# Optimization experiments

Hardware: AMD Instinct MI355X
Metric: run time of the kernel (lower is better)

The kernel has to match this reference:

```python
import jax, jax.numpy as jnp
import numpy as np

B, S, D, H, E, K = 4, 2048, 1024, 2048, 8, 2


def setup_inputs() -> dict:
    key = jax.random.key(0)
    ks = jax.random.split(key, 5)
    x = jax.random.normal(ks[0], (B, S, D), dtype=jnp.float32)
    Wr = jax.random.normal(ks[1], (D, E), dtype=jnp.float32) * 0.02  # router weight
    w1 = jax.random.normal(ks[2], (E, D, H), dtype=jnp.float32) * 0.02  # gate proj per expert
    w3 = jax.random.normal(ks[3], (E, D, H), dtype=jnp.float32) * 0.02  # up proj per expert
    w2 = jax.random.normal(ks[4], (E, H, D), dtype=jnp.float32) * 0.02  # down proj per expert
    return {"x": x, "Wr": Wr, "w1": w1, "w2": w2, "w3": w3}


def reference(x, Wr, w1, w2, w3):
    b, s, d = x.shape
    e = Wr.shape[1]
    flat = x.reshape(b * s, d)                      # [T, D]
    logits = flat @ Wr                              # [T, E]
    probs = jax.nn.softmax(logits, axis=-1)
    vals, idx = jax.lax.top_k(probs, K)             # [T, K]
    weights = vals / jnp.sum(vals, axis=-1, keepdims=True)
    onehot = jax.nn.one_hot(idx, e, dtype=flat.dtype)   # [T, K, E]
    cw = jnp.einsum('tke,tk->te', onehot, weights)      # combine weight per (token, expert)

    # naive dense: every expert computes every token, masked by combine weights
    out = jnp.zeros_like(flat)
    for ei in range(e):  # fixed small structural loop over experts
        h = jax.nn.silu(flat @ w1[ei]) * (flat @ w3[ei])   # [T, H]
        out = out + (h @ w2[ei]) * cw[:, ei:ei + 1]

    # aux load-balancing loss (usage uses any() over top-k slots, as in torch code)
    usage = (onehot.sum(axis=1) > 0).astype(flat.dtype).mean(axis=0)  # [E]
    prob_mass = probs.mean(axis=0)                                     # [E]
    aux_loss = e * jnp.sum(usage * prob_mass)
    return out.reshape(b, s, d), aux_loss
```

## Files before the change

### kernel.cpp

```cpp
#include <hip/hip_runtime.h>
#include <hip/hip_bf16.h>
#include <cstdint>
#include <cstddef>

#define T_TOK 8192
#define DIM   1024
#define HID   2048
#define NE    8
#define CAP   2816

typedef __attribute__((ext_vector_type(8))) short bf16x8;
typedef __attribute__((ext_vector_type(4))) float f32x4;
using bf16 = __hip_bfloat16;

__device__ __forceinline__ void gload16(const bf16* g, bf16* l) {
    __builtin_amdgcn_global_load_lds(
        (const __attribute__((address_space(1))) unsigned int*)(g),
        (__attribute__((address_space(3))) unsigned int*)(l), 16, 0, 0);
}
__device__ __forceinline__ float b2f(unsigned short u) {
    return __uint_as_float(((unsigned int)u) << 16);
}

__global__ void k_convert_x(const float* __restrict__ x, bf16* __restrict__ xb) {
    int i = (blockIdx.x * blockDim.x + threadIdx.x) * 4;
    float4 v = *(const float4*)(x + i);
    bf16 o[4] = {__float2bfloat16(v.x), __float2bfloat16(v.y),
                 __float2bfloat16(v.z), __float2bfloat16(v.w)};
    *(uint2*)(xb + i) = *(const uint2*)o;
}

__global__ __launch_bounds__(256) void k_transpose_bf16(const float* __restrict__ in,
                                                        bf16* __restrict__ out, int R, int C) {
    __shared__ float tile[64][65];
    int e = blockIdx.y;
    int ct = C >> 6;
    int r0 = (blockIdx.x / ct) << 6;
    int c0 = (blockIdx.x % ct) << 6;
    const float* src = in + (size_t)e * R * C;
    bf16* dst = out + (size_t)e * R * C;
    int s = threadIdx.x & 15, g = threadIdx.x >> 4;
#pragma unroll
    for (int j = 0; j < 4; ++j) {
        int row = j * 16 + g;
        float4 v = *(const float4*)(src + (size_t)(r0 + row) * C + c0 + s * 4);
        tile[row][s * 4 + 0] = v.x; tile[row][s * 4 + 1] = v.y;
        tile[row][s * 4 + 2] = v.z; tile[row][s * 4 + 3] = v.w;
    }
    __syncthreads();
#pragma unroll
    for (int j = 0; j < 4; ++j) {
        int c = j * 16 + g;
        int r = s * 4;
        bf16 o[4] = {__float2bfloat16(tile[r][c]),     __float2bfloat16(tile[r + 1][c]),
                     __float2bfloat16(tile[r + 2][c]), __float2bfloat16(tile[r + 3][c])};
        *(uint2*)(dst + (size_t)(c0 + c) * R + r0 + r) = *(const uint2*)o;
    }
}

__global__ __launch_bounds__(256) void k_logits(const float* __restrict__ x,
                                                const float* __restrict__ Wr,
                                                float* __restrict__ logits) {
    __shared__ float wl[NE][DIM];
    for (int o = threadIdx.x; o < NE * DIM; o += 256) {
        int e = o >> 10, d = o & (DIM - 1);
        wl[e][d] = Wr[d * NE + e];
    }
    __syncthreads();
    int wid = threadIdx.x >> 6, lane = threadIdx.x & 63;
    int t = blockIdx.x * 4 + wid;
    const float* xr = x + (size_t)t * DIM;
    double acc[NE];
#pragma unroll
    for (int e = 0; e < NE; ++e) acc[e] = 0.0;
    for (int i = 0; i < DIM / 64; ++i) {
        float xv = xr[i * 64 + lane];
#pragma unroll
        for (int e = 0; e < NE; ++e)
            acc[e] += (double)xv * (double)wl[e][i * 64 + lane];
    }
#pragma unroll
    for (int e = 0; e < NE; ++e) {
        double v = acc[e];
        for (int m = 32; m >= 1; m >>= 1) v += __shfl_xor(v, m);
        if (lane == 0) logits[t * NE + e] = (float)v;
    }
}

__global__ __launch_bounds__(256) void k_route(const float* __restrict__ logits,
                                               int* counts, int* seg_tok, float* seg_w,
                                               int* slotpos, float* probsum) {
    int t = blockIdx.x * 256 + threadIdx.x;
    float l[NE];
#pragma unroll
    for (int e = 0; e < NE; ++e) l[e] = logits[t * NE + e];
    float mx = l[0];
#pragma unroll
    for (int e = 1; e < NE; ++e) mx = fmaxf(mx, l[e]);
    float p[NE], s = 0.f;
#pragma unroll
    for (int e = 0; e < NE; ++e) { p[e] = expf(l[e] - mx); s += p[e]; }
    float inv = 1.f / s;
#pragma unroll
    for (int e = 0; e < NE; ++e) p[e] *= inv;
    int e0 = 0; float v0 = p[0];
#pragma unroll
    for (int e = 1; e < NE; ++e) if (p[e] > v0) { v0 = p[e]; e0 = e; }
    int e1 = -1; float v1 = -1.f;
#pragma unroll
    for (int e = 0; e < NE; ++e) if (e != e0 && p[e] > v1) { v1 = p[e]; e1 = e; }
    float wsum = v0 + v1;
    float w0 = v0 / wsum, w1 = v1 / wsum;

    int lane = threadIdx.x & 63, wid = threadIdx.x >> 6;
    __shared__ float ps[4][NE];
#pragma unroll
    for (int e = 0; e < NE; ++e) {
        float v = p[e];
        for (int m = 32; m >= 1; m >>= 1) v += __shfl_xor(v, m);
        if (lane == 0) ps[wid][e] = v;
    }
    __syncthreads();
    if (threadIdx.x < NE) {
        float v = ps[0][threadIdx.x] + ps[1][threadIdx.x] + ps[2][threadIdx.x] + ps[3][threadIdx.x];
        atomicAdd(&probsum[threadIdx.x], v);
    }
    for (int slot = 0; slot < 2; ++slot) {
        int   e  = slot ? e1 : e0;
        float wv = slot ? w1 : w0;
#pragma unroll
        for (int ex = 0; ex < NE; ++ex) {
            unsigned long long m = __ballot(e == ex);
            if (e == ex) {
                int leader = __ffsll(m) - 1;
                int base = 0;
                if (lane == leader) base = atomicAdd(&counts[ex], __popcll(m));
                base = __shfl(base, leader);
                int pos = base + (int)__popcll(m & ((1ull << lane) - 1ull));
                if (pos < CAP) {
                    seg_tok[ex * CAP + pos] = t;
                    seg_w[ex * CAP + pos]  = wv;
                    slotpos[2 * t + slot]  = ex * CAP + pos;
                } else {
                    slotpos[2 * t + slot]  = -1;
                }
            }
        }
    }
}

__global__ __launch_bounds__(256, 2) void k_gemm1(const bf16* __restrict__ xb,
                                                  const bf16* __restrict__ w1t,
                                                  const bf16* __restrict__ w3t,
                                                  const int* __restrict__ counts,
                                                  const int* __restrict__ seg_tok,
                                                  bf16* __restrict__ h) {
    __shared__ __align__(16) bf16 As[128 * 64];
    __shared__ __align__(16) bf16 Bg[128 * 64];
    __shared__ __align__(16) bf16 Bu[128 * 64];
    __shared__ int toks[128];
    const int NT = HID / 128;
    int flat = blockIdx.y * gridDim.x + blockIdx.x;
    int cpx  = (gridDim.x * NE) >> 3;
    int swz  = (flat & 7) * cpx + (flat >> 3);
    int e    = swz / gridDim.x;
    int tile = swz % gridDim.x;
    int mtile = tile / NT, ntile = tile % NT;
    int cnt = counts[e]; if (cnt > CAP) cnt = CAP;
    if (mtile * 128 >= cnt) return;

    int tx = threadIdx.x;
    if (tx < 128) {
        int slot = mtile * 128 + tx;
        toks[tx] = seg_tok[e * CAP + (slot < cnt ? slot : 0)];
    }
    __syncthreads();

    int lane = tx & 63, w = tx >> 6;
    const bf16 *ap[4], *gp[4], *up[4];
    bf16 *al[4], *gl[4], *ul[4];
#pragma unroll
    for (int i = 0; i < 4; ++i) {
        int seg = w * 4 + i;
        int r = seg * 8 + (lane >> 3);
        int co = (lane & 7) * 8;
        ap[i] = xb  + (size_t)toks[r] * DIM + co;
        gp[i] = w1t + ((size_t)e * HID + ntile * 128 + r) * DIM + co;
        up[i] = w3t + ((size_t)e * HID + ntile * 128 + r) * DIM + co;
        al[i] = As + seg * 512; gl[i] = Bg + seg * 512; ul[i] = Bu + seg * 512;
    }

    f32x4 zero4 = {0.f, 0.f, 0.f, 0.f};
    f32x4 accg[4][4], accu[4][4];
#pragma unroll
    for (int m = 0; m < 4; ++m)
#pragma unroll
        for (int n = 0; n < 4; ++n) { accg[m][n] = zero4; accu[m][n] = zero4; }
    int wr = w >> 1, wc = w & 1;

    for (int k0 = 0; k0 < DIM; k0 += 64) {
#pragma unroll
        for (int i = 0; i < 4; ++i) {
            gload16(ap[i] + k0, al[i]);
            gload16(gp[i] + k0, gl[i]);
            gload16(up[i] + k0, ul[i]);
        }
        __syncthreads();
#pragma unroll
        for (int ks = 0; ks < 2; ++ks) {
            bf16x8 af[4];
#pragma unroll
            for (int m = 0; m < 4; ++m)
                af[m] = *(const bf16x8*)(As + (wr * 64 + m * 16 + (lane & 15)) * 64 + ks * 32 + (lane >> 4) * 8);
#pragma unroll
            for (int n = 0; n < 4; ++n) {
                bf16x8 bgf = *(const bf16x8*)(Bg + (wc * 64 + n * 16 + (lane & 15)) * 64 + ks * 32 + (lane >> 4) * 8);
                bf16x8 buf_ = *(const bf16x8*)(Bu + (wc * 64 + n * 16 + (lane & 15)) * 64 + ks * 32 + (lane >> 4) * 8);
#pragma unroll
                for (int m = 0; m < 4; ++m) {
                    accg[m][n] = __builtin_amdgcn_mfma_f32_16x16x32_bf16(af[m], bgf, accg[m][n], 0, 0, 0);
                    accu[m][n] = __builtin_amdgcn_mfma_f32_16x16x32_bf16(af[m], buf_, accu[m][n], 0, 0, 0);
                }
            }
        }
        __syncthreads();
    }
    bf16* hdst = h + ((size_t)e * CAP + (size_t)mtile * 128) * HID + ntile * 128;
#pragma unroll
    for (int m = 0; m < 4; ++m)
#pragma unroll
        for (int n = 0; n < 4; ++n)
#pragma unroll
            for (int r = 0; r < 4; ++r) {
                int row = wr * 64 + m * 16 + (lane >> 4) * 4 + r;
                int col = wc * 64 + n * 16 + (lane & 15);
                float gg = accg[m][n][r], uu = accu[m][n][r];
                float hv = gg / (1.f + __expf(-gg)) * uu;
                hdst[(size_t)row * HID + col] = __float2bfloat16(hv);
            }
}

__global__ __launch_bounds__(256, 2) void k_gemm2(const bf16* __restrict__ h,
                                                  const bf16* __restrict__ w2t,
                                                  const int* __restrict__ counts,
                                                  const float* __restrict__ seg_w,
                                                  bf16* __restrict__ ybuf) {
    __shared__ __align__(16) bf16 As[128 * 64];
    __shared__ __align__(16) bf16 Bs[128 * 64];
    __shared__ float wts[128];
    const int NT = DIM / 128;
    int flat = blockIdx.y * gridDim.x + blockIdx.x;
    int cpx  = (gridDim.x * NE) >> 3;
    int swz  = (flat & 7) * cpx + (flat >> 3);
    int e    = swz / gridDim.x;
    int tile = swz % gridDim.x;
    int mtile = tile / NT, ntile = tile % NT;
    int cnt = counts[e]; if (cnt > CAP) cnt = CAP;
    if (mtile * 128 >= cnt) return;

    int tx = threadIdx.x;
    if (tx < 128) {
        int slot = mtile * 128 + tx;
        wts[tx] = (slot < cnt) ? seg_w[e * CAP + slot] : 0.f;
    }
    __syncthreads();

    int lane = tx & 63, w = tx >> 6;
    const bf16 *ap[4], *bp[4];
    bf16 *al[4], *bl[4];
#pragma unroll
    for (int i = 0; i < 4; ++i) {
        int seg = w * 4 + i;
        int r = seg * 8 + (lane >> 3);
        int co = (lane & 7) * 8;
        ap[i] = h   + ((size_t)e * CAP + mtile * 128 + r) * HID + co;
        bp[i] = w2t + ((size_t)e * DIM + ntile * 128 + r) * HID + co;
        al[i] = As + seg * 512; bl[i] = Bs + seg * 512;
    }

    f32x4 zero4 = {0.f, 0.f, 0.f, 0.f};
    f32x4 acc[4][4];
#pragma unroll
    for (int m = 0; m < 4; ++m)
#pragma unroll
        for (int n = 0; n < 4; ++n) acc[m][n] = zero4;
    int wr = w >> 1, wc = w & 1;

    for (int k0 = 0; k0 < HID; k0 += 64) {
#pragma unroll
        for (int i = 0; i < 4; ++i) {
            gload16(ap[i] + k0, al[i]);
            gload16(bp[i] + k0, bl[i]);
        }
        __syncthreads();
#pragma unroll
        for (int ks = 0; ks < 2; ++ks) {
            bf16x8 af[4];
#pragma unroll
            for (int m = 0; m < 4; ++m)
                af[m] = *(const bf16x8*)(As + (wr * 64 + m * 16 + (lane & 15)) * 64 + ks * 32 + (lane >> 4) * 8);
#pragma unroll
            for (int n = 0; n < 4; ++n) {
                bf16x8 b = *(const bf16x8*)(Bs + (wc * 64 + n * 16 + (lane & 15)) * 64 + ks * 32 + (lane >> 4) * 8);
#pragma unroll
                for (int m = 0; m < 4; ++m)
                    acc[m][n] = __builtin_amdgcn_mfma_f32_16x16x32_bf16(af[m], b, acc[m][n], 0, 0, 0);
            }
        }
        __syncthreads();
    }
    bf16* ydst = ybuf + ((size_t)e * CAP + (size_t)mtile * 128) * DIM + ntile * 128;
#pragma unroll
    for (int m = 0; m < 4; ++m)
#pragma unroll
        for (int n = 0; n < 4; ++n)
#pragma unroll
            for (int r = 0; r < 4; ++r) {
                int row = wr * 64 + m * 16 + (lane >> 4) * 4 + r;
                int col = wc * 64 + n * 16 + (lane & 15);
                ydst[(size_t)row * DIM + col] = __float2bfloat16(acc[m][n][r] * wts[row]);
            }
}

__global__ __launch_bounds__(256) void k_combine(const bf16* __restrict__ yb,
                                                 const int* __restrict__ slotpos,
                                                 float* __restrict__ out) {
    int t = blockIdx.x;
    int s0 = slotpos[2 * t], s1 = slotpos[2 * t + 1];
    int d = threadIdx.x * 4;
    float4 a = {0.f, 0.f, 0.f, 0.f};
    if (s0 >= 0) {
        ushort4 v = *(const ushort4*)(yb + (size_t)s0 * DIM + d);
        a.x += b2f(v.x); a.y += b2f(v.y); a.z += b2f(v.z); a.w += b2f(v.w);
    }
    if (s1 >= 0) {
        ushort4 v = *(const ushort4*)(yb + (size_t)s1 * DIM + d);
        a.x += b2f(v.x); a.y += b2f(v.y); a.z += b2f(v.z); a.w += b2f(v.w);
    }
    *(float4*)(out + (size_t)t * DIM + d) = a;
}

__global__ void k_aux(const int* __restrict__ counts, const float* __restrict__ probsum,
                      float* __restrict__ outaux) {
    if (threadIdx.x == 0 && blockIdx.x == 0) {
        float s = 0.f;
        for (int e = 0; e < NE; ++e)
            s += ((float)counts[e] / (float)T_TOK) * (probsum[e] / (float)T_TOK);
        *outaux = (float)NE * s;
    }
}

extern "C" void kernel_launch(void* const* d_in, const int* in_sizes, int n_in,
                              void* d_out, int out_size, void* d_ws, size_t ws_size,
                              hipStream_t stream) {
    const float* x  = (const float*)d_in[0];
    const float* Wr = (const float*)d_in[1];
    const float* w1 = (const float*)d_in[2];
    const float* w2 = (const float*)d_in[3];
    const float* w3 = (const float*)d_in[4];
    float* out = (float*)d_out;

    char* ws = (char*)d_ws;
    size_t off = 0;
    auto alloc = [&](size_t bytes) { void* p = ws + off; off += (bytes + 255) & ~(size_t)255; return p; };
    bf16*  xb      = (bf16*)alloc((size_t)T_TOK * DIM * 2);
    bf16*  w1t     = (bf16*)alloc((size_t)NE * HID * DIM * 2);
    bf16*  w3t     = (bf16*)alloc((size_t)NE * HID * DIM * 2);
    bf16*  w2t     = (bf16*)alloc((size_t)NE * DIM * HID * 2);
    bf16*  hbuf    = (bf16*)alloc((size_t)NE * CAP * HID * 2);
    float* logits  = (float*)alloc((size_t)T_TOK * NE * 4);
    int*   counts  = (int*)alloc(256);
    int*   segtok  = (int*)alloc((size_t)NE * CAP * 4);
    float* segw    = (float*)alloc((size_t)NE * CAP * 4);
    int*   slotpos = (int*)alloc((size_t)T_TOK * 2 * 4);
    float* probsum = (float*)alloc(256);
    bf16*  ybuf    = w1t;
    (void)ws_size; (void)in_sizes; (void)n_in;

    hipMemsetAsync(counts, 0, 256, stream);
    hipMemsetAsync(probsum, 0, 256, stream);

    k_convert_x<<<T_TOK * DIM / 4 / 256, 256, 0, stream>>>(x, xb);
    dim3 gt1((DIM / 64) * (HID / 64), NE);
    k_transpose_bf16<<<gt1, 256, 0, stream>>>(w1, w1t, DIM, HID);
    k_transpose_bf16<<<gt1, 256, 0, stream>>>(w3, w3t, DIM, HID);
    dim3 gt2((HID / 64) * (DIM / 64), NE);
    k_transpose_bf16<<<gt2, 256, 0, stream>>>(w2, w2t, HID, DIM);

    k_logits<<<T_TOK / 4, 256, 0, stream>>>(x, Wr, logits);
    k_route<<<T_TOK / 256, 256, 0, stream>>>(logits, counts, segtok, segw, slotpos, probsum);

    dim3 g1((CAP / 128) * (HID / 128), NE);
    k_gemm1<<<g1, 256, 0, stream>>>(xb, w1t, w3t, counts, segtok, hbuf);
    dim3 g2((CAP / 128) * (DIM / 128), NE);
    k_gemm2<<<g2, 256, 0, stream>>>(hbuf, w2t, counts, segw, ybuf);

    k_combine<<<T_TOK, 256, 0, stream>>>(ybuf, slotpos, out);
    k_aux<<<1, 64, 0, stream>>>(counts, probsum, out + (size_t)T_TOK * DIM);
}
```

Baseline: 439.2 us.

## Rewrite expert GEMMs with 3-stage LDS pipeline, swizzled tiles, 512-thread blocks

```diff
diff --git a/kernel.cpp b/kernel.cpp
--- a/kernel.cpp
+++ b/kernel.cpp
@@ -9,6 +9,8 @@
 #define NE    8
 #define CAP   2816
 
+#define SLOT  24576
+
 typedef __attribute__((ext_vector_type(8))) short bf16x8;
 typedef __attribute__((ext_vector_type(4))) float f32x4;
 using bf16 = __hip_bfloat16;
@@ -21,6 +23,10 @@
 __device__ __forceinline__ float b2f(unsigned short u) {
     return __uint_as_float(((unsigned int)u) << 16);
 }
+#define MFMA16(a, b, c) __builtin_amdgcn_mfma_f32_16x16x32_bf16((a), (b), (c), 0, 0, 0)
+#define BARRIER() asm volatile("s_barrier" ::: "memory")
+#define WAITVM6() asm volatile("s_waitcnt vmcnt(6)" ::: "memory")
+#define WAITVM0() asm volatile("s_waitcnt vmcnt(0)" ::: "memory")
 
 __global__ void k_convert_x(const float* __restrict__ x, bf16* __restrict__ xb) {
     int i = (blockIdx.x * blockDim.x + threadIdx.x) * 4;
@@ -149,177 +155,227 @@
     }
 }
 
-__global__ __launch_bounds__(256, 2) void k_gemm1(const bf16* __restrict__ xb,
+__global__ __launch_bounds__(512, 2) void k_gemm1(const bf16* __restrict__ xb,
                                                   const bf16* __restrict__ w1t,
                                                   const bf16* __restrict__ w3t,
                                                   const int* __restrict__ counts,
                                                   const int* __restrict__ seg_tok,
                                                   bf16* __restrict__ h) {
-    __shared__ __align__(16) bf16 As[128 * 64];
-    __shared__ __align__(16) bf16 Bg[128 * 64];
-    __shared__ __align__(16) bf16 Bu[128 * 64];
-    __shared__ int toks[128];
-    const int NT = HID / 128;
+    __shared__ __align__(16) bf16 lds[3 * SLOT];
+    __shared__ int toks[256];
+    const int NTL = HID / 64;
     int flat = blockIdx.y * gridDim.x + blockIdx.x;
     int cpx  = (gridDim.x * NE) >> 3;
     int swz  = (flat & 7) * cpx + (flat >> 3);
     int e    = swz / gridDim.x;
     int tile = swz % gridDim.x;
-    int mtile = tile / NT, ntile = tile % NT;
+    int mtile = tile / NTL, ntile = tile % NTL;
     int cnt = counts[e]; if (cnt > CAP) cnt = CAP;
-    if (mtile * 128 >= cnt) return;
-
-    int tx = threadIdx.x;
-    if (tx < 128) {
-        int slot = mtile * 128 + tx;
-        toks[tx] = seg_tok[e * CAP + (slot < cnt ? slot : 0)];
+    if (mtile * 256 >= cnt) return;
+
+    int tx = threadIdx.x, lane = tx & 63, wid = tx >> 6;
+    for (int i = tx; i < 256; i += 512) {
+        int slot = mtile * 256 + i;
+        toks[i] = seg_tok[e * CAP + (slot < cnt ? slot : 0)];
     }
     __syncthreads();
 
-    int lane = tx & 63, w = tx >> 6;
-    const bf16 *ap[4], *gp[4], *up[4];
-    bf16 *al[4], *gl[4], *ul[4];
-#pragma unroll
-    for (int i = 0; i < 4; ++i) {
-        int seg = w * 4 + i;
-        int r = seg * 8 + (lane >> 3);
-        int co = (lane & 7) * 8;
-        ap[i] = xb  + (size_t)toks[r] * DIM + co;
-        gp[i] = w1t + ((size_t)e * HID + ntile * 128 + r) * DIM + co;
-        up[i] = w3t + ((size_t)e * HID + ntile * 128 + r) * DIM + co;
-        al[i] = As + seg * 512; gl[i] = Bg + seg * 512; ul[i] = Bu + seg * 512;
-    }
-
+    int l3 = lane >> 3, l7 = lane & 7;
+    int swzco = (l7 ^ l3) << 3;
+    const bf16* ap0 = xb + (size_t)toks[  0 + wid * 8 + l3] * DIM + swzco;
+    const bf16* ap1 = xb + (size_t)toks[ 64 + wid * 8 + l3] * DIM + swzco;
+    const bf16* ap2 = xb + (size_t)toks[128 + wid * 8 + l3] * DIM + swzco;
+    const bf16* ap3 = xb + (size_t)toks[192 + wid * 8 + l3] * DIM + swzco;
+    const bf16* bgp = w1t + ((size_t)e * HID + ntile * 64 + wid * 8 + l3) * DIM + swzco;
+    const bf16* bup = w3t + ((size_t)e * HID + ntile * 64 + wid * 8 + l3) * DIM + swzco;
+    int wbase = wid * 512;
+
+    f32x4 accg[4][2], accu[4][2];
     f32x4 zero4 = {0.f, 0.f, 0.f, 0.f};
-    f32x4 accg[4][4], accu[4][4];
 #pragma unroll
     for (int m = 0; m < 4; ++m)
 #pragma unroll
-        for (int n = 0; n < 4; ++n) { accg[m][n] = zero4; accu[m][n] = zero4; }
-    int wr = w >> 1, wc = w & 1;
-
-    for (int k0 = 0; k0 < DIM; k0 += 64) {
-#pragma unroll
-        for (int i = 0; i < 4; ++i) {
-            gload16(ap[i] + k0, al[i]);
-            gload16(gp[i] + k0, gl[i]);
-            gload16(up[i] + k0, ul[i]);
-        }
-        __syncthreads();
-#pragma unroll
-        for (int ks = 0; ks < 2; ++ks) {
-            bf16x8 af[4];
-#pragma unroll
-            for (int m = 0; m < 4; ++m)
-                af[m] = *(const bf16x8*)(As + (wr * 64 + m * 16 + (lane & 15)) * 64 + ks * 32 + (lane >> 4) * 8);
-#pragma unroll
-            for (int n = 0; n < 4; ++n) {
-                bf16x8 bgf = *(const bf16x8*)(Bg + (wc * 64 + n * 16 + (lane & 15)) * 64 + ks * 32 + (lane >> 4) * 8);
-                bf16x8 buf_ = *(const bf16x8*)(Bu + (wc * 64 + n * 16 + (lane & 15)) * 64 + ks * 32 + (lane >> 4) * 8);
-#pragma unroll
-                for (int m = 0; m < 4; ++m) {
-                    accg[m][n] = __builtin_amdgcn_mfma_f32_16x16x32_bf16(af[m], bgf, accg[m][n], 0, 0, 0);
-                    accu[m][n] = __builtin_amdgcn_mfma_f32_16x16x32_bf16(af[m], buf_, accu[m][n], 0, 0, 0);
-                }
-            }
-        }
-        __syncthreads();
-    }
-    bf16* hdst = h + ((size_t)e * CAP + (size_t)mtile * 128) * HID + ntile * 128;
+        for (int n = 0; n < 2; ++n) { accg[m][n] = zero4; accu[m][n] = zero4; }
+
+    int wm = wid >> 1, wn = wid & 1;
+    int l15 = lane & 15, lh = lane >> 4;
+
+#define G1_STAGE_A(ss, ko) do { \
+        gload16(ap0 + (ko), lds + (ss) + 0 * 4096 + wbase); \
+        gload16(ap1 + (ko), lds + (ss) + 1 * 4096 + wbase); \
+        gload16(ap2 + (ko), lds + (ss) + 2 * 4096 + wbase); } while (0)
+#define G1_STAGE_B(ss, ko) do { \
+        gload16(ap3 + (ko), lds + (ss) + 3 * 4096 + wbase); \
+        gload16(bgp + (ko), lds + (ss) + 16384 + wbase); \
+        gload16(bup + (ko), lds + (ss) + 20480 + wbase); } while (0)
+#define G1_PHASE(cs, ph) do { \
+        int cex = ((((ph) << 2) + lh) ^ l7) << 3; \
+        bf16x8 a0 = *(const bf16x8*)(lds + (cs) + (wm * 64 +  0 + l15) * 64 + cex); \
+        bf16x8 a1 = *(const bf16x8*)(lds + (cs) + (wm * 64 + 16 + l15) * 64 + cex); \
+        bf16x8 a2 = *(const bf16x8*)(lds + (cs) + (wm * 64 + 32 + l15) * 64 + cex); \
+        bf16x8 a3 = *(const bf16x8*)(lds + (cs) + (wm * 64 + 48 + l15) * 64 + cex); \
+        bf16x8 g0 = *(const bf16x8*)(lds + (cs) + 16384 + (wn * 32 +  0 + l15) * 64 + cex); \
+        bf16x8 g1 = *(const bf16x8*)(lds + (cs) + 16384 + (wn * 32 + 16 + l15) * 64 + cex); \
+        bf16x8 u0 = *(const bf16x8*)(lds + (cs) + 20480 + (wn * 32 +  0 + l15) * 64 + cex); \
+        bf16x8 u1 = *(const bf16x8*)(lds + (cs) + 20480 + (wn * 32 + 16 + l15) * 64 + cex); \
+        __builtin_amdgcn_s_setprio(1); \
+        accg[0][0] = MFMA16(a0, g0, accg[0][0]); accg[1][0] = MFMA16(a1, g0, accg[1][0]); \
+        accg[2][0] = MFMA16(a2, g0, accg[2][0]); accg[3][0] = MFMA16(a3, g0, accg[3][0]); \
+        accg[0][1] = MFMA16(a0, g1, accg[0][1]); accg[1][1] = MFMA16(a1, g1, accg[1][1]); \
+        accg[2][1] = MFMA16(a2, g1, accg[2][1]); accg[3][1] = MFMA16(a3, g1, accg[3][1]); \
+        accu[0][0] = MFMA16(a0, u0, accu[0][0]); accu[1][0] = MFMA16(a1, u0, accu[1][0]); \
+        accu[2][0] = MFMA16(a2, u0, accu[2][0]); accu[3][0] = MFMA16(a3, u0, accu[3][0]); \
+        accu[0][1] = MFMA16(a0, u1, accu[0][1]); accu[1][1] = MFMA16(a1, u1, accu[1][1]); \
+        accu[2][1] = MFMA16(a2, u1, accu[2][1]); accu[3][1] = MFMA16(a3, u1, accu[3][1]); \
+        __builtin_amdgcn_s_setprio(0); } while (0)
+
+    G1_STAGE_A(0, 0);    G1_STAGE_B(0, 0);
+    G1_STAGE_A(SLOT, 64); G1_STAGE_B(SLOT, 64);
+
+    const int NT = DIM / 64;
+    int cs = 0, ss = 2 * SLOT, ko = 128;
+#pragma unroll 1
+    for (int T = 0; T < NT; ++T) {
+        bool st = (T + 2 < NT);
+        if (T == NT - 1) WAITVM0(); else WAITVM6();
+        BARRIER();
+        if (st) G1_STAGE_A(ss, ko);
+        G1_PHASE(cs, 0);
+        BARRIER();
+        if (st) G1_STAGE_B(ss, ko);
+        G1_PHASE(cs, 1);
+        cs += SLOT; if (cs == 3 * SLOT) cs = 0;
+        ss += SLOT; if (ss == 3 * SLOT) ss = 0;
+        ko += 64;
+    }
+
+    bf16* hdst = h + ((size_t)e * CAP + (size_t)mtile * 256) * HID + ntile * 64;
 #pragma unroll
     for (int m = 0; m < 4; ++m)
 #pragma unroll
-        for (int n = 0; n < 4; ++n)
+        for (int n = 0; n < 2; ++n)
 #pragma unroll
             for (int r = 0; r < 4; ++r) {
-                int row = wr * 64 + m * 16 + (lane >> 4) * 4 + r;
-                int col = wc * 64 + n * 16 + (lane & 15);
+                int row = wm * 64 + m * 16 + lh * 4 + r;
+                int col = wn * 32 + n * 16 + l15;
                 float gg = accg[m][n][r], uu = accu[m][n][r];
                 float hv = gg / (1.f + __expf(-gg)) * uu;
                 hdst[(size_t)row * HID + col] = __float2bfloat16(hv);
             }
-}
-
-__global__ __launch_bounds__(256, 2) void k_gemm2(const bf16* __restrict__ h,
+#undef G1_STAGE_A
+#undef G1_STAGE_B
+#undef G1_PHASE
+}
+
+__global__ __launch_bounds__(512, 2) void k_gemm2(const bf16* __restrict__ h,
                                                   const bf16* __restrict__ w2t,
                                                   const int* __restrict__ counts,
                                                   const float* __restrict__ seg_w,
                                                   bf16* __restrict__ ybuf) {
-    __shared__ __align__(16) bf16 As[128 * 64];
-    __shared__ __align__(16) bf16 Bs[128 * 64];
-    __shared__ float wts[128];
-    const int NT = DIM / 128;
+    __shared__ __align__(16) bf16 lds[3 * SLOT];
+    __shared__ float wts[256];
+    const int NTL = DIM / 128;
     int flat = blockIdx.y * gridDim.x + blockIdx.x;
     int cpx  = (gridDim.x * NE) >> 3;
     int swz  = (flat & 7) * cpx + (flat >> 3);
     int e    = swz / gridDim.x;
     int tile = swz % gridDim.x;
-    int mtile = tile / NT, ntile = tile % NT;
+    int mtile = tile / NTL, ntile = tile % NTL;
     int cnt = counts[e]; if (cnt > CAP) cnt = CAP;
-    if (mtile * 128 >= cnt) return;
-
-    int tx = threadIdx.x;
-    if (tx < 128) {
-        int slot = mtile * 128 + tx;
-        wts[tx] = (slot < cnt) ? seg_w[e * CAP + slot] : 0.f;
+    if (mtile * 256 >= cnt) return;
+
+    int tx = threadIdx.x, lane = tx & 63, wid = tx >> 6;
+    for (int i = tx; i < 256; i += 512) {
+        int slot = mtile * 256 + i;
+        wts[i] = (slot < cnt) ? seg_w[e * CAP + slot] : 0.f;
     }
     __syncthreads();
 
-    int lane = tx & 63, w = tx >> 6;
-    const bf16 *ap[4], *bp[4];
-    bf16 *al[4], *bl[4];
-#pragma unroll
-    for (int i = 0; i < 4; ++i) {
-        int seg = w * 4 + i;
-        int r = seg * 8 + (lane >> 3);
-        int co = (lane & 7) * 8;
-        ap[i] = h   + ((size_t)e * CAP + mtile * 128 + r) * HID + co;
-        bp[i] = w2t + ((size_t)e * DIM + ntile * 128 + r) * HID + co;
-        al[i] = As + seg * 512; bl[i] = Bs + seg * 512;
-    }
-
+    int l3 = lane >> 3, l7 = lane & 7;
+    int swzco = (l7 ^ l3) << 3;
+    const bf16* ap0 = h + ((size_t)e * CAP + mtile * 256 +   0 + wid * 8 + l3) * HID + swzco;
+    const bf16* ap1 = h + ((size_t)e * CAP + mtile * 256 +  64 + wid * 8 + l3) * HID + swzco;
+    const bf16* ap2 = h + ((size_t)e * CAP + mtile * 256 + 128 + wid * 8 + l3) * HID + swzco;
+    const bf16* ap3 = h + ((size_t)e * CAP + mtile * 256 + 192 + wid * 8 + l3) * HID + swzco;
+    const bf16* bp0 = w2t + ((size_t)e * DIM + ntile * 128 +  0 + wid * 8 + l3) * HID + swzco;
+    const bf16* bp1 = w2t + ((size_t)e * DIM + ntile * 128 + 64 + wid * 8 + l3) * HID + swzco;
+    int wbase = wid * 512;
+
+    f32x4 acc[8][2];
     f32x4 zero4 = {0.f, 0.f, 0.f, 0.f};
-    f32x4 acc[4][4];
-#pragma unroll
-    for (int m = 0; m < 4; ++m)
-#pragma unroll
-        for (int n = 0; n < 4; ++n) acc[m][n] = zero4;
-    int wr = w >> 1, wc = w & 1;
-
-    for (int k0 = 0; k0 < HID; k0 += 64) {
-#pragma unroll
-        for (int i = 0; i < 4; ++i) {
-            gload16(ap[i] + k0, al[i]);
-            gload16(bp[i] + k0, bl[i]);
-        }
-        __syncthreads();
-#pragma unroll
-        for (int ks = 0; ks < 2; ++ks) {
-            bf16x8 af[4];
-#pragma unroll
-            for (int m = 0; m < 4; ++m)
-                af[m] = *(const bf16x8*)(As + (wr * 64 + m * 16 + (lane & 15)) * 64 + ks * 32 + (lane >> 4) * 8);
-#pragma unroll
-            for (int n = 0; n < 4; ++n) {
-                bf16x8 b = *(const bf16x8*)(Bs + (wc * 64 + n * 16 + (lane & 15)) * 64 + ks * 32 + (lane >> 4) * 8);
-#pragma unroll
-                for (int m = 0; m < 4; ++m)
-                    acc[m][n] = __builtin_amdgcn_mfma_f32_16x16x32_bf16(af[m], b, acc[m][n], 0, 0, 0);
-            }
-        }
-        __syncthreads();
-    }
-    bf16* ydst = ybuf + ((size_t)e * CAP + (size_t)mtile * 128) * DIM + ntile * 128;
-#pragma unroll
-    for (int m = 0; m < 4; ++m)
-#pragma unroll
-        for (int n = 0; n < 4; ++n)
+#pragma unroll
+    for (int m = 0; m < 8; ++m)
+#pragma unroll
+        for (int n = 0; n < 2; ++n) acc[m][n] = zero4;
+
+    int wm = wid >> 2, wn = wid & 3;
+    int l15 = lane & 15, lh = lane >> 4;
+
+#define G2_STAGE_A(ss, ko) do { \
+        gload16(ap0 + (ko), lds + (ss) + 0 * 4096 + wbase); \
+        gload16(ap1 + (ko), lds + (ss) + 1 * 4096 + wbase); \
+        gload16(ap2 + (ko), lds + (ss) + 2 * 4096 + wbase); } while (0)
+#define G2_STAGE_B(ss, ko) do { \
+        gload16(ap3 + (ko), lds + (ss) + 3 * 4096 + wbase); \
+        gload16(bp0 + (ko), lds + (ss) + 16384 + wbase); \
+        gload16(bp1 + (ko), lds + (ss) + 20480 + wbase); } while (0)
+#define G2_PHASE(cs, ph) do { \
+        int cex = ((((ph) << 2) + lh) ^ l7) << 3; \
+        bf16x8 b0 = *(const bf16x8*)(lds + (cs) + 16384 + (wn * 32 +  0 + l15) * 64 + cex); \
+        bf16x8 b1 = *(const bf16x8*)(lds + (cs) + 16384 + (wn * 32 + 16 + l15) * 64 + cex); \
+        bf16x8 a0 = *(const bf16x8*)(lds + (cs) + (wm * 128 +   0 + l15) * 64 + cex); \
+        bf16x8 a1 = *(const bf16x8*)(lds + (cs) + (wm * 128 +  16 + l15) * 64 + cex); \
+        bf16x8 a2 = *(const bf16x8*)(lds + (cs) + (wm * 128 +  32 + l15) * 64 + cex); \
+        bf16x8 a3 = *(const bf16x8*)(lds + (cs) + (wm * 128 +  48 + l15) * 64 + cex); \
+        bf16x8 a4 = *(const bf16x8*)(lds + (cs) + (wm * 128 +  64 + l15) * 64 + cex); \
+        bf16x8 a5 = *(const bf16x8*)(lds + (cs) + (wm * 128 +  80 + l15) * 64 + cex); \
+        bf16x8 a6 = *(const bf16x8*)(lds + (cs) + (wm * 128 +  96 + l15) * 64 + cex); \
+        bf16x8 a7 = *(const bf16x8*)(lds + (cs) + (wm * 128 + 112 + l15) * 64 + cex); \
+        __builtin_amdgcn_s_setprio(1); \
+        acc[0][0] = MFMA16(a0, b0, acc[0][0]); acc[1][0] = MFMA16(a1, b0, acc[1][0]); \
+        acc[2][0] = MFMA16(a2, b0, acc[2][0]); acc[3][0] = MFMA16(a3, b0, acc[3][0]); \
+        acc[4][0] = MFMA16(a4, b0, acc[4][0]); acc[5][0] = MFMA16(a5, b0, acc[5][0]); \
+        acc[6][0] = MFMA16(a6, b0, acc[6][0]); acc[7][0] = MFMA16(a7, b0, acc[7][0]); \
+        acc[0][1] = MFMA16(a0, b1, acc[0][1]); acc[1][1] = MFMA16(a1, b1, acc[1][1]); \
+        acc[2][1] = MFMA16(a2, b1, acc[2][1]); acc[3][1] = MFMA16(a3, b1, acc[3][1]); \
+        acc[4][1] = MFMA16(a4, b1, acc[4][1]); acc[5][1] = MFMA16(a5, b1, acc[5][1]); \
+        acc[6][1] = MFMA16(a6, b1, acc[6][1]); acc[7][1] = MFMA16(a7, b1, acc[7][1]); \
+        __builtin_amdgcn_s_setprio(0); } while (0)
+
+    G2_STAGE_A(0, 0);     G2_STAGE_B(0, 0);
+    G2_STAGE_A(SLOT, 64); G2_STAGE_B(SLOT, 64);
+
+    const int NT = HID / 64;
+    int cs = 0, ss = 2 * SLOT, ko = 128;
+#pragma unroll 1
+    for (int T = 0; T < NT; ++T) {
+        bool st = (T + 2 < NT);
+        if (T == NT - 1) WAITVM0(); else WAITVM6();
+        BARRIER();
+        if (st) G2_STAGE_A(ss, ko);
+        G2_PHASE(cs, 0);
+        BARRIER();
+        if (st) G2_STAGE_B(ss, ko);
+        G2_PHASE(cs, 1);
+        cs += SLOT; if (cs == 3 * SLOT) cs = 0;
+        ss += SLOT; if (ss == 3 * SLOT) ss = 0;
+        ko += 64;
+    }
+
+    bf16* ydst = ybuf + ((size_t)e * CAP + (size_t)mtile * 256) * DIM + ntile * 128;
+#pragma unroll
+    for (int m = 0; m < 8; ++m)
+#pragma unroll
+        for (int n = 0; n < 2; ++n)
 #pragma unroll
             for (int r = 0; r < 4; ++r) {
-                int row = wr * 64 + m * 16 + (lane >> 4) * 4 + r;
-                int col = wc * 64 + n * 16 + (lane & 15);
+                int row = wm * 128 + m * 16 + lh * 4 + r;
+                int col = wn * 32 + n * 16 + l15;
                 ydst[(size_t)row * DIM + col] = __float2bfloat16(acc[m][n][r] * wts[row]);
             }
+#undef G2_STAGE_A
+#undef G2_STAGE_B
+#undef G2_PHASE
 }
 
 __global__ __launch_bounds__(256) void k_combine(const bf16* __restrict__ yb,
@@ -390,10 +446,10 @@
     k_logits<<<T_TOK / 4, 256, 0, stream>>>(x, Wr, logits);
     k_route<<<T_TOK / 256, 256, 0, stream>>>(logits, counts, segtok, segw, slotpos, probsum);
 
-    dim3 g1((CAP / 128) * (HID / 128), NE);
-    k_gemm1<<<g1, 256, 0, stream>>>(xb, w1t, w3t, counts, segtok, hbuf);
-    dim3 g2((CAP / 128) * (DIM / 128), NE);
-    k_gemm2<<<g2, 256, 0, stream>>>(hbuf, w2t, counts, segw, ybuf);
+    dim3 g1((CAP / 256) * (HID / 64), NE);
+    k_gemm1<<<g1, 512, 0, stream>>>(xb, w1t, w3t, counts, segtok, hbuf);
+    dim3 g2((CAP / 256) * (DIM / 128), NE);
+    k_gemm2<<<g2, 512, 0, stream>>>(hbuf, w2t, counts, segw, ybuf);
 
     k_combine<<<T_TOK, 256, 0, stream>>>(ybuf, slotpos, out);
     k_aux<<<1, 64, 0, stream>>>(counts, probsum, out + (size_t)T_TOK * DIM);
```

Result: slower. 611.7 us (+39.3%).
